# Performance work log

Measured on AMD Instinct MI355X. Metric: run time of the kernel, lower is better.

Reference implementation:

```python
import math
import jax, jax.numpy as jnp
import numpy as np

NUM_SUPERPIXELS = 256
COMPACTNESS = 10.0
NUM_ITERATIONS = 5


def _cdist(a, b):
    # Euclidean pairwise distance: a [B,N,C], b [B,K,C] -> [B,N,K]
    a2 = jnp.sum(a * a, axis=-1)[:, :, None]
    b2 = jnp.sum(b * b, axis=-1)[:, None, :]
    ab = jnp.einsum('bnc,bkc->bnk', a, b)
    return jnp.sqrt(jnp.maximum(a2 + b2 - 2.0 * ab, 1e-12))


def setup_inputs() -> dict:
    key = jax.random.key(0)
    x = jax.random.normal(key, (4, 200, 128, 128), dtype=jnp.float32)
    return {"x": x}


def reference(x):
    B, C, H, W = x.shape
    N = H * W

    # --- initialize_centers (grid of seed pixels, taken from x[0]) ---
    grid_h = int(math.sqrt(NUM_SUPERPIXELS * H / W))
    grid_w = NUM_SUPERPIXELS // grid_h
    K = grid_h * grid_w
    h_step, w_step = H // grid_h, W // grid_w
    h_idx = jnp.arange(h_step // 2, H, h_step)[:grid_h]
    w_idx = jnp.arange(w_step // 2, W, w_step)[:grid_w]
    gy, gx = jnp.meshgrid(h_idx, w_idx, indexing='ij')
    init_spatial = jnp.stack([gy.flatten(), gx.flatten()], axis=1).astype(jnp.float32)  # [K,2]
    flat_idx = gy.flatten() * W + gx.flatten()  # [K]

    # --- pixel coordinates ---
    yg, xg = jnp.meshgrid(jnp.arange(H), jnp.arange(W), indexing='ij')
    pix = jnp.stack([yg.flatten(), xg.flatten()], axis=1).astype(jnp.float32)  # [N,2]
    pix_b = jnp.broadcast_to(pix[None], (B, N, 2))

    x_flat = jnp.transpose(x, (0, 2, 3, 1)).reshape(B, N, C)  # [B,N,C]
    centers_spectral = jnp.broadcast_to(x_flat[0][flat_idx][None], (B, K, C))
    centers_spatial = jnp.broadcast_to(init_spatial[None], (B, K, 2))

    S = math.sqrt(H * W / NUM_SUPERPIXELS)
    Q = None
    for _ in range(NUM_ITERATIONS):
        D = _cdist(x_flat, centers_spectral) + (COMPACTNESS / S) * _cdist(pix_b, centers_spatial)
        Q = jax.nn.softmax(-D, axis=-1)  # [B,N,K]
        mass = jnp.sum(Q, axis=1)[:, :, None] + 1e-06  # [B,K,1]
        centers_spectral = jnp.einsum('bnk,bnc->bkc', Q, x_flat) / mass
        centers_spatial = jnp.einsum('bnk,bnc->bkc', Q, pix_b) / mass
    return Q, centers_spectral
```

## Files before the change

kernel.cpp:

```cpp
#include <hip/hip_runtime.h>
#include <math.h>

#define B 4
#define C 200
#define H 128
#define W 128
#define N 16384
#define K 256
#define ITERS 5
#define FACT 1.25f
#define NT 32
#define NTM 128
#define CPAD 208

typedef __attribute__((ext_vector_type(8))) __bf16 bf16x8;
typedef __attribute__((ext_vector_type(4))) float f32x4;

#define OFF_A2    0
#define OFF_CS    (OFF_A2 + B*N)
#define OFF_CSPAT (OFF_CS + B*K*C)
#define OFF_B2    (OFF_CSPAT + B*K*2)
#define OFF_SACC  (OFF_B2 + B*K)
#define OFF_MACC  (OFF_SACC + B*K*C)
#define OFF_SPACC (OFF_MACC + B*K)
#define OFF_CST   (OFF_SPACC + B*K*2)
#define CST_SZ    (B*C*K)
#define OFF_PART  (OFF_CST + CST_SZ)
#define PART_SZ   (B*NT*CPAD*K)
#define OFF_MPART (OFF_PART + PART_SZ)
#define MPART_SZ  (B*NTM*3*K)
#define WS_NEED   ((size_t)(OFF_MPART + MPART_SZ) * 4)

__global__ void k_init(const float* __restrict__ x, float* __restrict__ cs,
                       float* __restrict__ cst, float* __restrict__ cspat) {
  int k = blockIdx.x, c = threadIdx.x;
  int i = k >> 4, j = k & 15;
  int sn = (4 + 8*i)*W + (4 + 8*j);
  if (c < C) {
    float v = x[(size_t)c*N + sn];
    for (int b = 0; b < B; ++b) {
      cs[((size_t)(b*K + k))*C + c] = v;
      cst[((size_t)(b*C + c))*K + k] = v;
    }
  }
  if (c == 0) {
    for (int b = 0; b < B; ++b) {
      cspat[(b*K + k)*2 + 0] = (float)(4 + 8*i);
      cspat[(b*K + k)*2 + 1] = (float)(4 + 8*j);
    }
  }
}

__global__ void k_a2(const float* __restrict__ x, float* __restrict__ a2) {
  int b = blockIdx.x >> 6;
  int n = ((blockIdx.x & 63) << 8) + threadIdx.x;
  const float* xp = x + (size_t)b*C*N + n;
  float s = 0.f;
  #pragma unroll 8
  for (int c = 0; c < C; ++c) { float v = xp[(size_t)c*N]; s += v*v; }
  a2[b*N + n] = s;
}

__global__ void k_b2(const float* __restrict__ cs, float* __restrict__ b2) {
  int bk = blockIdx.x;
  const float* p = cs + (size_t)bk*C;
  float s = 0.f;
  for (int c = threadIdx.x; c < C; c += 64) { float v = p[c]; s += v*v; }
  for (int off = 32; off > 0; off >>= 1) s += __shfl_down(s, off);
  if (threadIdx.x == 0) b2[bk] = s;
}

__global__ __launch_bounds__(512, 2) void k_assign(
    const float* __restrict__ x, const float* __restrict__ cs,
    const float* __restrict__ cspat, const float* __restrict__ b2,
    const float* __restrict__ a2, float* __restrict__ Q) {
  __shared__ __bf16 cs_lds[K*40];
  __shared__ __bf16 x_lds[128*40];
  __shared__ float b2s[K], cys[K], cxs[K];
  __shared__ float a2s[128];
  __shared__ float redw[8*128];
  __shared__ float redf[128];

  int b   = blockIdx.x >> 7;
  int n0  = (blockIdx.x & 127) << 7;
  int tid = threadIdx.x;
  int lane = tid & 63;
  int lr = lane & 15;
  int lg = lane >> 4;
  int w  = tid >> 6;

  if (tid < K) {
    b2s[tid] = b2[b*K + tid];
    cys[tid] = cspat[(b*K + tid)*2 + 0];
    cxs[tid] = cspat[(b*K + tid)*2 + 1];
  }
  if (tid < 128) a2s[tid] = a2[b*N + n0 + tid];

  f32x4 acc[16];
  #pragma unroll
  for (int i = 0; i < 16; ++i) acc[i] = (f32x4){0.f, 0.f, 0.f, 0.f};

  const float* xb = x + (size_t)b*C*N;
  const float* cb = cs + (size_t)b*K*C;

  for (int t = 0; t < 7; ++t) {
    int cc0 = t * 32;
    __syncthreads();
    #pragma unroll
    for (int pass = 0; pass < 4; ++pass) {
      int f = pass*512 + tid;
      int k = f >> 3, c4 = (f & 7) * 4;
      float4 v = make_float4(0.f, 0.f, 0.f, 0.f);
      if (cc0 + c4 < 200) v = *(const float4*)&cb[(size_t)k*C + cc0 + c4];
      __bf16* d = &cs_lds[k*40 + c4];
      d[0] = (__bf16)v.x; d[1] = (__bf16)v.y;
      d[2] = (__bf16)v.z; d[3] = (__bf16)v.w;
    }
    #pragma unroll
    for (int pass = 0; pass < 8; ++pass) {
      int idx = pass*512 + tid;
      int ci = idx >> 7, p = idx & 127;
      float xv = (cc0 + ci < 200) ? xb[(size_t)(cc0 + ci)*N + n0 + p] : 0.f;
      x_lds[p*40 + ci] = (__bf16)xv;
    }
    __syncthreads();
    const __bf16* bbase = &cs_lds[(w*32 + lr)*40 + lg*8];
    bf16x8 b0 = *(const bf16x8*)bbase;
    bf16x8 b1 = *(const bf16x8*)(bbase + 16*40);
    const __bf16* abase = &x_lds[lr*40 + lg*8];
    #pragma unroll
    for (int nt = 0; nt < 8; ++nt) {
      bf16x8 av = *(const bf16x8*)(abase + nt*16*40);
      acc[nt*2+0] = __builtin_amdgcn_mfma_f32_16x16x32_bf16(av, b0, acc[nt*2+0], 0, 0, 0);
      acc[nt*2+1] = __builtin_amdgcn_mfma_f32_16x16x32_bf16(av, b1, acc[nt*2+1], 0, 0, 0);
    }
  }

  float py = (float)(n0 >> 7);
  float mArr[32];
  #pragma unroll
  for (int nt = 0; nt < 8; ++nt) {
    #pragma unroll
    for (int r = 0; r < 4; ++r) {
      int pix = nt*16 + lg*4 + r;
      float a2v = a2s[pix];
      float pxv = (float)pix;
      float dmin = 1e30f;
      #pragma unroll
      for (int j = 0; j < 2; ++j) {
        int k = w*32 + j*16 + lr;
        float ab = acc[nt*2+j][r];
        float dy = py - cys[k];
        float dx = pxv - cxs[k];
        float d = sqrtf(fmaxf(a2v + b2s[k] - 2.f*ab, 1e-12f))
                + FACT*sqrtf(fmaxf(dy*dy + dx*dx, 1e-12f));
        acc[nt*2+j][r] = d;
        dmin = fminf(dmin, d);
      }
      mArr[nt*4+r] = dmin;
    }
  }
  #pragma unroll
  for (int i = 0; i < 32; ++i) {
    float m = mArr[i];
    m = fminf(m, __shfl_xor(m, 1));
    m = fminf(m, __shfl_xor(m, 2));
    m = fminf(m, __shfl_xor(m, 4));
    m = fminf(m, __shfl_xor(m, 8));
    mArr[i] = m;
  }
  if (lr == 0) {
    #pragma unroll
    for (int nt = 0; nt < 8; ++nt)
      #pragma unroll
      for (int r = 0; r < 4; ++r)
        redw[w*128 + nt*16 + lg*4 + r] = mArr[nt*4+r];
  }
  __syncthreads();
  if (tid < 128) {
    float m = redw[tid];
    #pragma unroll
    for (int g = 1; g < 8; ++g) m = fminf(m, redw[g*128 + tid]);
    redf[tid] = m;
  }
  __syncthreads();
  #pragma unroll
  for (int nt = 0; nt < 8; ++nt) {
    #pragma unroll
    for (int r = 0; r < 4; ++r) {
      int pix = nt*16 + lg*4 + r;
      float mnv = redf[pix];
      float s = 0.f;
      #pragma unroll
      for (int j = 0; j < 2; ++j) {
        float e = __expf(mnv - acc[nt*2+j][r]);
        acc[nt*2+j][r] = e;
        s += e;
      }
      s += __shfl_xor(s, 1);
      s += __shfl_xor(s, 2);
      s += __shfl_xor(s, 4);
      s += __shfl_xor(s, 8);
      mArr[nt*4+r] = s;
    }
  }
  if (lr == 0) {
    #pragma unroll
    for (int nt = 0; nt < 8; ++nt)
      #pragma unroll
      for (int r = 0; r < 4; ++r)
        redw[w*128 + nt*16 + lg*4 + r] = mArr[nt*4+r];
  }
  __syncthreads();
  if (tid < 128) {
    float s = redw[tid];
    #pragma unroll
    for (int g = 1; g < 8; ++g) s += redw[g*128 + tid];
    redf[tid] = 1.f / s;
  }
  __syncthreads();
  float* Qb = Q + ((size_t)(b*N + n0))*K;
  #pragma unroll
  for (int nt = 0; nt < 8; ++nt) {
    #pragma unroll
    for (int r = 0; r < 4; ++r) {
      int pix = nt*16 + lg*4 + r;
      float inv = redf[pix];
      #pragma unroll
      for (int j = 0; j < 2; ++j) {
        int k = w*32 + j*16 + lr;
        Qb[(size_t)pix*K + k] = acc[nt*2+j][r] * inv;
      }
    }
  }
}

__global__ __launch_bounds__(256) void k_update4(
    const float* __restrict__ x, const float* __restrict__ Q,
    float* __restrict__ part) {
  __shared__ float  q32[32*256];
  __shared__ __bf16 qbf[256*40];
  __shared__ __bf16 xbf[64*40];
  int bid = blockIdx.x;
  int b   = bid >> 7;
  int rem = bid & 127;
  int cg  = rem >> 5;
  int nt  = rem & 31;
  int tid = threadIdx.x;
  int lane = tid & 63, lr = lane & 15, lg = lane >> 4;
  int w   = tid >> 6;
  int c0  = cg * 64;

  f32x4 acc[16];
  #pragma unroll
  for (int i = 0; i < 16; ++i) acc[i] = (f32x4){0.f, 0.f, 0.f, 0.f};

  const float* Qb = Q + (size_t)b*N*K;
  const float* xb = x + (size_t)b*C*N;

  for (int ch = 0; ch < 16; ++ch) {
    int nb = nt*512 + ch*32;
    __syncthreads();
    #pragma unroll
    for (int pass = 0; pass < 8; ++pass) {
      int f = pass*256 + tid;
      int n = f >> 6, k4 = f & 63;
      *(float4*)&q32[n*256 + k4*4] =
          *(const float4*)&Qb[(size_t)(nb + n)*K + k4*4];
    }
    #pragma unroll
    for (int pass = 0; pass < 2; ++pass) {
      int f = pass*256 + tid;
      int c = f >> 3, n4 = f & 7;
      int cc = c0 + c;
      float4 v = make_float4(0.f, 0.f, 0.f, 0.f);
      if (cc < 200) v = *(const float4*)&xb[(size_t)cc*N + nb + n4*4];
      __bf16* d = &xbf[c*40 + n4*4];
      d[0] = (__bf16)v.x; d[1] = (__bf16)v.y;
      d[2] = (__bf16)v.z; d[3] = (__bf16)v.w;
    }
    __syncthreads();
    {
      #pragma unroll
      for (int g = 0; g < 4; ++g) {
        bf16x8 pk;
        #pragma unroll
        for (int i = 0; i < 8; ++i)
          pk[i] = (__bf16)q32[(g*8 + i)*256 + tid];
        *(bf16x8*)&qbf[tid*40 + g*8] = pk;
      }
    }
    __syncthreads();
    const __bf16* abase = &qbf[(w*64 + lr)*40 + lg*8];
    const __bf16* bbase = &xbf[lr*40 + lg*8];
    bf16x8 A0 = *(const bf16x8*)(abase);
    bf16x8 A1 = *(const bf16x8*)(abase + 16*40);
    bf16x8 A2 = *(const bf16x8*)(abase + 32*40);
    bf16x8 A3 = *(const bf16x8*)(abase + 48*40);
    bf16x8 B0 = *(const bf16x8*)(bbase);
    bf16x8 B1 = *(const bf16x8*)(bbase + 16*40);
    bf16x8 B2 = *(const bf16x8*)(bbase + 32*40);
    bf16x8 B3 = *(const bf16x8*)(bbase + 48*40);
    acc[0]  = __builtin_amdgcn_mfma_f32_16x16x32_bf16(A0, B0, acc[0], 0, 0, 0);
    acc[1]  = __builtin_amdgcn_mfma_f32_16x16x32_bf16(A0, B1, acc[1], 0, 0, 0);
    acc[2]  = __builtin_amdgcn_mfma_f32_16x16x32_bf16(A0, B2, acc[2], 0, 0, 0);
    acc[3]  = __builtin_amdgcn_mfma_f32_16x16x32_bf16(A0, B3, acc[3], 0, 0, 0);
    acc[4]  = __builtin_amdgcn_mfma_f32_16x16x32_bf16(A1, B0, acc[4], 0, 0, 0);
    acc[5]  = __builtin_amdgcn_mfma_f32_16x16x32_bf16(A1, B1, acc[5], 0, 0, 0);
    acc[6]  = __builtin_amdgcn_mfma_f32_16x16x32_bf16(A1, B2, acc[6], 0, 0, 0);
    acc[7]  = __builtin_amdgcn_mfma_f32_16x16x32_bf16(A1, B3, acc[7], 0, 0, 0);
    acc[8]  = __builtin_amdgcn_mfma_f32_16x16x32_bf16(A2, B0, acc[8], 0, 0, 0);
    acc[9]  = __builtin_amdgcn_mfma_f32_16x16x32_bf16(A2, B1, acc[9], 0, 0, 0);
    acc[10] = __builtin_amdgcn_mfma_f32_16x16x32_bf16(A2, B2, acc[10], 0, 0, 0);
    acc[11] = __builtin_amdgcn_mfma_f32_16x16x32_bf16(A2, B3, acc[11], 0, 0, 0);
    acc[12] = __builtin_amdgcn_mfma_f32_16x16x32_bf16(A3, B0, acc[12], 0, 0, 0);
    acc[13] = __builtin_amdgcn_mfma_f32_16x16x32_bf16(A3, B1, acc[13], 0, 0, 0);
    acc[14] = __builtin_amdgcn_mfma_f32_16x16x32_bf16(A3, B2, acc[14], 0, 0, 0);
    acc[15] = __builtin_amdgcn_mfma_f32_16x16x32_bf16(A3, B3, acc[15], 0, 0, 0);
  }

  float* pp = part + (size_t)(b*NT + nt) * CPAD * K;
  #pragma unroll
  for (int t = 0; t < 4; ++t) {
    #pragma unroll
    for (int u = 0; u < 4; ++u) {
      int c = c0 + u*16 + lr;
      if (c < CPAD) {
        int k = w*64 + t*16 + lg*4;
        *(f32x4*)&pp[(size_t)c*K + k] = acc[t*4+u];
      }
    }
  }
}

__global__ __launch_bounds__(256) void k_mass(
    const float* __restrict__ Q, float* __restrict__ mpart) {
  int bid = blockIdx.x;
  int b = bid >> 7, nt = bid & 127;
  int tid = threadIdx.x;
  const float* Qb = Q + (size_t)b*N*K;
  int nbase = nt * 128;
  float mass = 0.f, sy = 0.f, sx = 0.f;
  for (int nn = 0; nn < 128; nn += 8) {
    float qv[8];
    #pragma unroll
    for (int j = 0; j < 8; ++j)
      qv[j] = Qb[(size_t)(nbase + nn + j)*K + tid];
    #pragma unroll
    for (int j = 0; j < 8; ++j) {
      int n = nbase + nn + j;
      mass += qv[j];
      sy += qv[j] * (float)(n >> 7);
      sx += qv[j] * (float)(n & 127);
    }
  }
  float* mp = mpart + (size_t)(b*NTM + nt) * 3 * K;
  mp[tid]       = mass;
  mp[K + tid]   = sy;
  mp[2*K + tid] = sx;
}

__global__ __launch_bounds__(256) void k_reduce(
    const float* __restrict__ part, const float* __restrict__ mpart,
    float* __restrict__ sacc, float* __restrict__ macc,
    float* __restrict__ spacc) {
  int bid = blockIdx.x;
  int b = bid / 200;
  int c = bid % 200;
  int tid = threadIdx.x;
  float s = 0.f;
  for (int nt = 0; nt < NT; ++nt)
    s += part[((size_t)(b*NT + nt)*CPAD + c)*K + tid];
  sacc[(size_t)(b*K + tid)*C + c] = s;
  if (c == 0) {
    float m = 0.f, yy = 0.f, xx = 0.f;
    for (int nt = 0; nt < NTM; ++nt) {
      const float* mp = mpart + (size_t)(b*NTM + nt) * 3 * K;
      m  += mp[tid];
      yy += mp[K + tid];
      xx += mp[2*K + tid];
    }
    macc[b*K + tid] = m;
    spacc[(b*K + tid)*2 + 0] = yy;
    spacc[(b*K + tid)*2 + 1] = xx;
  }
}

__global__ __launch_bounds__(256, 2) void k_update(
    const float* __restrict__ x, const float* __restrict__ Q,
    float* __restrict__ sacc, float* __restrict__ macc,
    float* __restrict__ spacc) {
  __shared__ float x_lds[32*28];
  int bid = blockIdx.x;
  int b = bid >> 9;
  int rest = bid & 511;
  int ct = rest >> 6;
  int nt = rest & 63;
  int tid = threadIdx.x;
  int c0 = ct * 25;

  float acc[25];
  #pragma unroll
  for (int c = 0; c < 25; ++c) acc[c] = 0.f;
  float mass = 0.f, sy = 0.f, sx = 0.f;

  const float* xb = x + (size_t)b*C*N + (size_t)c0*N;
  const float* Qb = Q + (size_t)b*N*K;

  for (int ch = 0; ch < 8; ++ch) {
    int nb = nt*256 + ch*32;
    __syncthreads();
    #pragma unroll
    for (int pass = 0; pass < 4; ++pass) {
      int idx = pass*256 + tid;
      if (idx < 800) {
        int ci = idx >> 5, nn = idx & 31;
        x_lds[nn*28 + ci] = xb[(size_t)ci*N + nb + nn];
      }
    }
    __syncthreads();
    float py  = (float)(nb >> 7);
    float pxb = (float)(nb & 127);
    #pragma unroll
    for (int n4 = 0; n4 < 8; ++n4) {
      float qv[4];
      #pragma unroll
      for (int j = 0; j < 4; ++j)
        qv[j] = Qb[(size_t)(nb + n4*4 + j)*K + tid];
      #pragma unroll
      for (int j = 0; j < 4; ++j) {
        int nn = n4*4 + j;
        float q = qv[j];
        if (ct == 0) {
          mass += q;
          sy += q * py;
          sx += q * (pxb + (float)nn);
        }
        const float* xr = &x_lds[nn*28];
        #pragma unroll
        for (int c4 = 0; c4 < 6; ++c4) {
          float4 xv = *(const float4*)&xr[c4*4];
          acc[c4*4+0] = fmaf(q, xv.x, acc[c4*4+0]);
          acc[c4*4+1] = fmaf(q, xv.y, acc[c4*4+1]);
          acc[c4*4+2] = fmaf(q, xv.z, acc[c4*4+2]);
          acc[c4*4+3] = fmaf(q, xv.w, acc[c4*4+3]);
        }
        acc[24] = fmaf(q, xr[24], acc[24]);
      }
    }
  }
  float* sp = sacc + ((size_t)(b*K + tid))*C + c0;
  #pragma unroll
  for (int c = 0; c < 25; ++c) atomicAdd(&sp[c], acc[c]);
  if (ct == 0) {
    atomicAdd(&macc[b*K + tid], mass);
    atomicAdd(&spacc[(b*K + tid)*2 + 0], sy);
    atomicAdd(&spacc[(b*K + tid)*2 + 1], sx);
  }
}

__global__ void k_final(const float* __restrict__ sacc, const float* __restrict__ macc,
                        const float* __restrict__ spacc, float* __restrict__ cs,
                        float* __restrict__ cst, float* __restrict__ cspat,
                        float* __restrict__ b2, float* __restrict__ outc, int last) {
  __shared__ float red[256];
  int bk = blockIdx.x;
  int b = bk >> 8, kk = bk & 255;
  int c = threadIdx.x;
  float inv = 1.f / (macc[bk] + 1e-6f);
  float v = 0.f;
  if (c < C) {
    v = sacc[(size_t)bk*C + c] * inv;
    cs[(size_t)bk*C + c] = v;
    cst[((size_t)(b*C + c))*K + kk] = v;
    if (last) outc[(size_t)bk*C + c] = v;
  } else if (c == C) {
    cspat[bk*2 + 0] = spacc[bk*2 + 0] * inv;
  } else if (c == C + 1) {
    cspat[bk*2 + 1] = spacc[bk*2 + 1] * inv;
  }
  red[c] = v * v;
  __syncthreads();
  for (int off = 128; off > 0; off >>= 1) {
    if (c < off) red[c] += red[c + off];
    __syncthreads();
  }
  if (c == 0) b2[bk] = red[0];
}

extern "C" void kernel_launch(void* const* d_in, const int* in_sizes, int n_in,
                              void* d_out, int out_size, void* d_ws, size_t ws_size,
                              hipStream_t stream) {
  const float* x = (const float*)d_in[0];
  float* out = (float*)d_out;
  float* ws  = (float*)d_ws;
  float* a2    = ws + OFF_A2;
  float* cs    = ws + OFF_CS;
  float* cspat = ws + OFF_CSPAT;
  float* b2    = ws + OFF_B2;
  float* sacc  = ws + OFF_SACC;
  float* macc  = ws + OFF_MACC;
  float* spacc = ws + OFF_SPACC;
  float* cst   = ws + OFF_CST;
  float* part  = ws + OFF_PART;
  float* mpart = ws + OFF_MPART;
  float* outc  = out + (size_t)B*N*K;
  int split = (ws_size >= WS_NEED) ? 1 : 0;

  hipLaunchKernelGGL(k_init, dim3(K), dim3(256), 0, stream, x, cs, cst, cspat);
  hipLaunchKernelGGL(k_a2, dim3(B*64), dim3(256), 0, stream, x, a2);
  hipLaunchKernelGGL(k_b2, dim3(B*K), dim3(64), 0, stream, cs, b2);
  for (int it = 0; it < ITERS; ++it) {
    hipLaunchKernelGGL(k_assign, dim3(B*128), dim3(512), 0, stream,
                       x, cs, cspat, b2, a2, out);
    if (split) {
      hipLaunchKernelGGL(k_update4, dim3(B*4*NT), dim3(256), 0, stream,
                         x, out, part);
      hipLaunchKernelGGL(k_mass, dim3(B*NTM), dim3(256), 0, stream,
                         out, mpart);
      hipLaunchKernelGGL(k_reduce, dim3(B*200), dim3(256), 0, stream,
                         part, mpart, sacc, macc, spacc);
    } else {
      hipMemsetAsync(sacc, 0, (size_t)(B*K*C + B*K + B*K*2)*sizeof(float), stream);
      hipLaunchKernelGGL(k_update, dim3(B*512), dim3(256), 0, stream,
                         x, out, sacc, macc, spacc);
    }
    hipLaunchKernelGGL(k_final, dim3(B*K), dim3(256), 0, stream,
                       sacc, macc, spacc, cs, cst, cspat, b2, outc,
                       (it == ITERS-1) ? 1 : 0);
  }
}
```

Before: 668.5 us.

## Precompute bf16 pixel-major x and centers to feed assign MFMA directly

Adds a one-time prep kernel that transposes x into a pixel-major bf16 buffer padded to 224 channels. Centers are also kept as padded bf16 rows, written by init and final in place of the transposed fp32 copy. A new assign kernel loads these tiles straight into LDS with vector loads, which avoids per-iteration strided fp32 reads and conversion. This depends on a larger workspace, and the path falls back when the workspace is too small.

```diff
diff --git a/kernel.cpp b/kernel.cpp
--- a/kernel.cpp
+++ b/kernel.cpp
@@ -12,6 +12,7 @@
 #define NT 32
 #define NTM 128
 #define CPAD 208
+#define CP2  224
 
 typedef __attribute__((ext_vector_type(8))) __bf16 bf16x8;
 typedef __attribute__((ext_vector_type(4))) float f32x4;
@@ -30,9 +31,15 @@
 #define OFF_MPART (OFF_PART + PART_SZ)
 #define MPART_SZ  (B*NTM*3*K)
 #define WS_NEED   ((size_t)(OFF_MPART + MPART_SZ) * 4)
+#define OFF_XBF   (OFF_MPART + MPART_SZ)
+#define XBF_SZF   (B*N*CP2/2)
+#define OFF_CSBF  (OFF_XBF + XBF_SZF)
+#define CSBF_SZF  (B*K*CP2/2)
+#define WS_NEED2  ((size_t)(OFF_CSBF + CSBF_SZF) * 4)
 
 __global__ void k_init(const float* __restrict__ x, float* __restrict__ cs,
-                       float* __restrict__ cst, float* __restrict__ cspat) {
+                       __bf16* __restrict__ csbf, float* __restrict__ cspat,
+                       int fast) {
   int k = blockIdx.x, c = threadIdx.x;
   int i = k >> 4, j = k & 15;
   int sn = (4 + 8*i)*W + (4 + 8*j);
@@ -40,13 +47,47 @@
     float v = x[(size_t)c*N + sn];
     for (int b = 0; b < B; ++b) {
       cs[((size_t)(b*K + k))*C + c] = v;
-      cst[((size_t)(b*C + c))*K + k] = v;
-    }
+      if (fast) csbf[((size_t)(b*K + k))*CP2 + c] = (__bf16)v;
+    }
+  } else if (fast && c < CP2) {
+    for (int b = 0; b < B; ++b)
+      csbf[((size_t)(b*K + k))*CP2 + c] = (__bf16)0.f;
   }
   if (c == 0) {
     for (int b = 0; b < B; ++b) {
       cspat[(b*K + k)*2 + 0] = (float)(4 + 8*i);
       cspat[(b*K + k)*2 + 1] = (float)(4 + 8*j);
+    }
+  }
+}
+
+__global__ __launch_bounds__(256) void k_prep(const float* __restrict__ x,
+                                              __bf16* __restrict__ xbf) {
+  __shared__ float xt[32*64];
+  int bid = blockIdx.x;
+  int b  = bid >> 8;
+  int n0 = (bid & 255) << 6;
+  int tid = threadIdx.x;
+  const float* xb = x + (size_t)b*C*N;
+  __bf16* xo = xbf + ((size_t)b*N + n0)*CP2;
+  for (int t = 0; t < 7; ++t) {
+    int cc0 = t*32;
+    __syncthreads();
+    #pragma unroll
+    for (int pass = 0; pass < 2; ++pass) {
+      int f = pass*256 + tid;
+      int ci = f >> 4, nq = f & 15;
+      float4 v = make_float4(0.f, 0.f, 0.f, 0.f);
+      if (cc0 + ci < C) v = *(const float4*)&xb[(size_t)(cc0 + ci)*N + n0 + nq*4];
+      *(float4*)&xt[ci*64 + nq*4] = v;
+    }
+    __syncthreads();
+    {
+      int n = tid & 63, cg8 = (tid >> 6) * 8;
+      bf16x8 pk;
+      #pragma unroll
+      for (int i = 0; i < 8; ++i) pk[i] = (__bf16)xt[(cg8 + i)*64 + n];
+      *(bf16x8*)&xo[(size_t)n*CP2 + cc0 + cg8] = pk;
     }
   }
 }
@@ -68,6 +109,166 @@
   for (int c = threadIdx.x; c < C; c += 64) { float v = p[c]; s += v*v; }
   for (int off = 32; off > 0; off >>= 1) s += __shfl_down(s, off);
   if (threadIdx.x == 0) b2[bk] = s;
+}
+
+__global__ __launch_bounds__(512, 2) void k_assign2(
+    const __bf16* __restrict__ xbf, const __bf16* __restrict__ csbf,
+    const float* __restrict__ cspat, const float* __restrict__ b2,
+    const float* __restrict__ a2, float* __restrict__ Q) {
+  __shared__ __bf16 cs_lds[K*40];
+  __shared__ __bf16 x_lds[128*40];
+  __shared__ float b2s[K], cys[K], cxs[K];
+  __shared__ float a2s[128];
+  __shared__ float redw[8*128];
+  __shared__ float redf[128];
+
+  int b   = blockIdx.x >> 7;
+  int n0  = (blockIdx.x & 127) << 7;
+  int tid = threadIdx.x;
+  int lane = tid & 63;
+  int lr = lane & 15;
+  int lg = lane >> 4;
+  int w  = tid >> 6;
+
+  if (tid < K) {
+    b2s[tid] = b2[b*K + tid];
+    cys[tid] = cspat[(b*K + tid)*2 + 0];
+    cxs[tid] = cspat[(b*K + tid)*2 + 1];
+  }
+  if (tid < 128) a2s[tid] = a2[b*N + n0 + tid];
+
+  f32x4 acc[16];
+  #pragma unroll
+  for (int i = 0; i < 16; ++i) acc[i] = (f32x4){0.f, 0.f, 0.f, 0.f};
+
+  const __bf16* cb = csbf + (size_t)b*K*CP2;
+  const __bf16* xb = xbf + ((size_t)b*N + n0)*CP2;
+
+  for (int t = 0; t < 7; ++t) {
+    int cc0 = t * 32;
+    __syncthreads();
+    #pragma unroll
+    for (int pass = 0; pass < 2; ++pass) {
+      int f = pass*512 + tid;
+      int k = f >> 2, j = f & 3;
+      *(bf16x8*)&cs_lds[k*40 + j*8] =
+          *(const bf16x8*)&cb[(size_t)k*CP2 + cc0 + j*8];
+    }
+    {
+      int p = tid >> 2, j = tid & 3;
+      *(bf16x8*)&x_lds[p*40 + j*8] =
+          *(const bf16x8*)&xb[(size_t)p*CP2 + cc0 + j*8];
+    }
+    __syncthreads();
+    const __bf16* bbase = &cs_lds[(w*32 + lr)*40 + lg*8];
+    bf16x8 b0 = *(const bf16x8*)bbase;
+    bf16x8 b1 = *(const bf16x8*)(bbase + 16*40);
+    const __bf16* abase = &x_lds[lr*40 + lg*8];
+    #pragma unroll
+    for (int nt = 0; nt < 8; ++nt) {
+      bf16x8 av = *(const bf16x8*)(abase + nt*16*40);
+      acc[nt*2+0] = __builtin_amdgcn_mfma_f32_16x16x32_bf16(av, b0, acc[nt*2+0], 0, 0, 0);
+      acc[nt*2+1] = __builtin_amdgcn_mfma_f32_16x16x32_bf16(av, b1, acc[nt*2+1], 0, 0, 0);
+    }
+  }
+
+  float py = (float)(n0 >> 7);
+  float mArr[32];
+  #pragma unroll
+  for (int nt = 0; nt < 8; ++nt) {
+    #pragma unroll
+    for (int r = 0; r < 4; ++r) {
+      int pix = nt*16 + lg*4 + r;
+      float a2v = a2s[pix];
+      float pxv = (float)pix;
+      float dmin = 1e30f;
+      #pragma unroll
+      for (int j = 0; j < 2; ++j) {
+        int k = w*32 + j*16 + lr;
+        float ab = acc[nt*2+j][r];
+        float dy = py - cys[k];
+        float dx = pxv - cxs[k];
+        float d = sqrtf(fmaxf(a2v + b2s[k] - 2.f*ab, 1e-12f))
+                + FACT*sqrtf(fmaxf(dy*dy + dx*dx, 1e-12f));
+        acc[nt*2+j][r] = d;
+        dmin = fminf(dmin, d);
+      }
+      mArr[nt*4+r] = dmin;
+    }
+  }
+  #pragma unroll
+  for (int i = 0; i < 32; ++i) {
+    float m = mArr[i];
+    m = fminf(m, __shfl_xor(m, 1));
+    m = fminf(m, __shfl_xor(m, 2));
+    m = fminf(m, __shfl_xor(m, 4));
+    m = fminf(m, __shfl_xor(m, 8));
+    mArr[i] = m;
+  }
+  if (lr == 0) {
+    #pragma unroll
+    for (int nt = 0; nt < 8; ++nt)
+      #pragma unroll
+      for (int r = 0; r < 4; ++r)
+        redw[w*128 + nt*16 + lg*4 + r] = mArr[nt*4+r];
+  }
+  __syncthreads();
+  if (tid < 128) {
+    float m = redw[tid];
+    #pragma unroll
+    for (int g = 1; g < 8; ++g) m = fminf(m, redw[g*128 + tid]);
+    redf[tid] = m;
+  }
+  __syncthreads();
+  #pragma unroll
+  for (int nt = 0; nt < 8; ++nt) {
+    #pragma unroll
+    for (int r = 0; r < 4; ++r) {
+      int pix = nt*16 + lg*4 + r;
+      float mnv = redf[pix];
+      float s = 0.f;
+      #pragma unroll
+      for (int j = 0; j < 2; ++j) {
+        float e = __expf(mnv - acc[nt*2+j][r]);
+        acc[nt*2+j][r] = e;
+        s += e;
+      }
+      s += __shfl_xor(s, 1);
+      s += __shfl_xor(s, 2);
+      s += __shfl_xor(s, 4);
+      s += __shfl_xor(s, 8);
+      mArr[nt*4+r] = s;
+    }
+  }
+  if (lr == 0) {
+    #pragma unroll
+    for (int nt = 0; nt < 8; ++nt)
+      #pragma unroll
+      for (int r = 0; r < 4; ++r)
+        redw[w*128 + nt*16 + lg*4 + r] = mArr[nt*4+r];
+  }
+  __syncthreads();
+  if (tid < 128) {
+    float s = redw[tid];
+    #pragma unroll
+    for (int g = 1; g < 8; ++g) s += redw[g*128 + tid];
+    redf[tid] = 1.f / s;
+  }
+  __syncthreads();
+  float* Qb = Q + ((size_t)(b*N + n0))*K;
+  #pragma unroll
+  for (int nt = 0; nt < 8; ++nt) {
+    #pragma unroll
+    for (int r = 0; r < 4; ++r) {
+      int pix = nt*16 + lg*4 + r;
+      float inv = redf[pix];
+      #pragma unroll
+      for (int j = 0; j < 2; ++j) {
+        int k = w*32 + j*16 + lr;
+        Qb[(size_t)pix*K + k] = acc[nt*2+j][r] * inv;
+      }
+    }
+  }
 }
 
 __global__ __launch_bounds__(512, 2) void k_assign(
@@ -461,18 +662,18 @@
 
 __global__ void k_final(const float* __restrict__ sacc, const float* __restrict__ macc,
                         const float* __restrict__ spacc, float* __restrict__ cs,
-                        float* __restrict__ cst, float* __restrict__ cspat,
-                        float* __restrict__ b2, float* __restrict__ outc, int last) {
+                        __bf16* __restrict__ csbf, float* __restrict__ cspat,
+                        float* __restrict__ b2, float* __restrict__ outc,
+                        int last, int fast) {
   __shared__ float red[256];
   int bk = blockIdx.x;
-  int b = bk >> 8, kk = bk & 255;
   int c = threadIdx.x;
   float inv = 1.f / (macc[bk] + 1e-6f);
   float v = 0.f;
   if (c < C) {
     v = sacc[(size_t)bk*C + c] * inv;
     cs[(size_t)bk*C + c] = v;
-    cst[((size_t)(b*C + c))*K + kk] = v;
+    if (fast) csbf[(size_t)bk*CP2 + c] = (__bf16)v;
     if (last) outc[(size_t)bk*C + c] = v;
   } else if (c == C) {
     cspat[bk*2 + 0] = spacc[bk*2 + 0] * inv;
@@ -501,18 +702,26 @@
   float* sacc  = ws + OFF_SACC;
   float* macc  = ws + OFF_MACC;
   float* spacc = ws + OFF_SPACC;
-  float* cst   = ws + OFF_CST;
   float* part  = ws + OFF_PART;
   float* mpart = ws + OFF_MPART;
+  __bf16* xbf  = (__bf16*)(ws + OFF_XBF);
+  __bf16* csbf = (__bf16*)(ws + OFF_CSBF);
   float* outc  = out + (size_t)B*N*K;
   int split = (ws_size >= WS_NEED) ? 1 : 0;
-
-  hipLaunchKernelGGL(k_init, dim3(K), dim3(256), 0, stream, x, cs, cst, cspat);
+  int fast  = (ws_size >= WS_NEED2) ? 1 : 0;
+
+  hipLaunchKernelGGL(k_init, dim3(K), dim3(256), 0, stream, x, cs, csbf, cspat, fast);
   hipLaunchKernelGGL(k_a2, dim3(B*64), dim3(256), 0, stream, x, a2);
   hipLaunchKernelGGL(k_b2, dim3(B*K), dim3(64), 0, stream, cs, b2);
+  if (fast)
+    hipLaunchKernelGGL(k_prep, dim3(B*256), dim3(256), 0, stream, x, xbf);
   for (int it = 0; it < ITERS; ++it) {
-    hipLaunchKernelGGL(k_assign, dim3(B*128), dim3(512), 0, stream,
-                       x, cs, cspat, b2, a2, out);
+    if (fast)
+      hipLaunchKernelGGL(k_assign2, dim3(B*128), dim3(512), 0, stream,
+                         xbf, csbf, cspat, b2, a2, out);
+    else
+      hipLaunchKernelGGL(k_assign, dim3(B*128), dim3(512), 0, stream,
+                         x, cs, cspat, b2, a2, out);
     if (split) {
       hipLaunchKernelGGL(k_update4, dim3(B*4*NT), dim3(256), 0, stream,
                          x, out, part);
@@ -526,7 +735,7 @@
                          x, out, sacc, macc, spacc);
     }
     hipLaunchKernelGGL(k_final, dim3(B*K), dim3(256), 0, stream,
-                       sacc, macc, spacc, cs, cst, cspat, b2, outc,
-                       (it == ITERS-1) ? 1 : 0);
-  }
-}
+                       sacc, macc, spacc, cs, csbf, cspat, b2, outc,
+                       (it == ITERS-1) ? 1 : 0, fast);
+  }
+}
```

After: 729.9 us. +9.2%, slower.
